# Performance work log

Hardware: AMD Instinct MI355X
Metric: run time of the kernel (lower is better)

The kernel has to match this reference:

```python
import jax, jax.numpy as jnp
import numpy as np

N = 100000
E = 1600000
G = 128


def _degrees(src, dst, n):
    ones = jnp.ones(src.shape[0], dtype=jnp.float32)
    deg_out = jax.ops.segment_sum(ones, src, num_segments=n)
    deg_in = jax.ops.segment_sum(ones, dst, num_segments=n)
    return jnp.maximum(deg_out, 1.0), jnp.maximum(deg_in, 1.0)


def gcn_conv(x, W, b, src, dst, norm_out, norm_in):
    # DGL GraphConv, norm='both': scale src by d_out^-1/2, sum over edges,
    # scale dst by d_in^-1/2, then linear. Weight applied first (out<=in) --
    # mathematically identical, cheaper gather.
    h = (x * norm_out[:, None]) @ W          # [N, out]
    m = h[src]                               # [E, out] gather
    agg = jax.ops.segment_sum(m, dst, num_segments=N)  # [N, out] scatter-add
    return agg * norm_in[:, None] + b


def setup_inputs() -> dict:
    key = jax.random.key(0)
    ks = jax.random.split(key, 8)
    x = jax.random.normal(ks[0], (N, 128), dtype=jnp.float32)
    W1 = jax.random.normal(ks[1], (128, 64), dtype=jnp.float32) * (1.0 / np.sqrt(128))
    b1 = jnp.zeros((64,), dtype=jnp.float32)
    W2 = jax.random.normal(ks[2], (64, 16), dtype=jnp.float32) * (1.0 / np.sqrt(64))
    b2 = jnp.zeros((16,), dtype=jnp.float32)
    src = jax.random.randint(ks[3], (E,), 0, N, dtype=jnp.int32)
    dst = jax.random.randint(ks[4], (E,), 0, N, dtype=jnp.int32)
    graph_ids = jnp.sort(jax.random.randint(ks[5], (N,), 0, G, dtype=jnp.int32))
    return {"x": x, "W1": W1, "b1": b1, "W2": W2, "b2": b2,
            "src": src, "dst": dst, "graph_ids": graph_ids}


def reference(x, W1, b1, W2, b2, src, dst, graph_ids):
    deg_out, deg_in = _degrees(src, dst, N)
    norm_out = jax.lax.rsqrt(deg_out)
    norm_in = jax.lax.rsqrt(deg_in)
    h = gcn_conv(x, W1, b1, src, dst, norm_out, norm_in)
    h = jax.nn.relu(h)
    # dropout(p=0.2) is identity in eval mode
    h = gcn_conv(h, W2, b2, src, dst, norm_out, norm_in)
    # dgl.mean_nodes: per-graph mean pooling
    sums = jax.ops.segment_sum(h, graph_ids, num_segments=G)      # [G, 16]
    counts = jax.ops.segment_sum(jnp.ones((N,), jnp.float32), graph_ids, num_segments=G)
    return sums / jnp.maximum(counts, 1.0)[:, None]
```

## Files before the change

kernel.cpp:

```cpp
#include <hip/hip_runtime.h>
#include <hip/hip_fp16.h>

#define N_NODES 100000
#define N_EDGES 1600000
#define N_GRAPHS 128
#define SB 391
#define CAP 4608
#define NBLK 512
#define NE4 (N_EDGES / 4)
#define CH4 782
#define LDX 136

typedef unsigned long long u64;
typedef unsigned int u32;
typedef unsigned char u8;
typedef _Float16 f16;
typedef f16 half8 __attribute__((ext_vector_type(8)));
typedef f16 half4v __attribute__((ext_vector_type(4)));
typedef float floatx4 __attribute__((ext_vector_type(4)));

__global__ void k_init(int* __restrict__ cur_d, int* __restrict__ cur_s) {
  int t = blockIdx.x * blockDim.x + threadIdx.x;
  if (t < SB) { cur_d[t] = t * CAP; cur_s[t] = t * CAP; }
}

__global__ __launch_bounds__(256) void k_fuse(const int4* __restrict__ src4,
                                              const int4* __restrict__ dst4,
                                              int* __restrict__ cur_d,
                                              int* __restrict__ cur_s,
                                              u32* __restrict__ ed,
                                              u8* __restrict__ ssk8) {
  __shared__ int hd[SB], hs[SB], ld[SB], ls[SB];
  const int t = threadIdx.x, b = blockIdx.x;
  for (int j = t; j < SB; j += 256) { hd[j] = 0; hs[j] = 0; }
  __syncthreads();
  const int start = b * CH4, end = min(start + CH4, NE4);
  for (int i = start + t; i < end; i += 256) {
    int4 d = dst4[i]; int4 s = src4[i];
    atomicAdd(&hd[d.x >> 8], 1); atomicAdd(&hd[d.y >> 8], 1);
    atomicAdd(&hd[d.z >> 8], 1); atomicAdd(&hd[d.w >> 8], 1);
    atomicAdd(&hs[s.x >> 8], 1); atomicAdd(&hs[s.y >> 8], 1);
    atomicAdd(&hs[s.z >> 8], 1); atomicAdd(&hs[s.w >> 8], 1);
  }
  __syncthreads();
  for (int j = t; j < SB; j += 256) {
    ld[j] = atomicAdd(&cur_d[j], hd[j]);
    ls[j] = atomicAdd(&cur_s[j], hs[j]);
  }
  __syncthreads();
  for (int i = start + t; i < end; i += 256) {
    int4 d4 = dst4[i]; int4 s4 = src4[i];
    {
      int d = d4.x, s = s4.x;
      int pd = atomicAdd(&ld[d >> 8], 1);
      ed[pd] = ((u32)(d & 255) << 24) | (u32)s;
      int ps = atomicAdd(&ls[s >> 8], 1);
      ssk8[ps] = (u8)(s & 255);
    }
    {
      int d = d4.y, s = s4.y;
      int pd = atomicAdd(&ld[d >> 8], 1);
      ed[pd] = ((u32)(d & 255) << 24) | (u32)s;
      int ps = atomicAdd(&ls[s >> 8], 1);
      ssk8[ps] = (u8)(s & 255);
    }
    {
      int d = d4.z, s = s4.z;
      int pd = atomicAdd(&ld[d >> 8], 1);
      ed[pd] = ((u32)(d & 255) << 24) | (u32)s;
      int ps = atomicAdd(&ls[s >> 8], 1);
      ssk8[ps] = (u8)(s & 255);
    }
    {
      int d = d4.w, s = s4.w;
      int pd = atomicAdd(&ld[d >> 8], 1);
      ed[pd] = ((u32)(d & 255) << 24) | (u32)s;
      int ps = atomicAdd(&ls[s >> 8], 1);
      ssk8[ps] = (u8)(s & 255);
    }
  }
}

__global__ __launch_bounds__(256) void k_bucket_csr(const u32* __restrict__ ed,
                                                    const u8* __restrict__ ssk8,
                                                    const int* __restrict__ cur_d,
                                                    const int* __restrict__ cur_s,
                                                    int* __restrict__ row_ptr,
                                                    int* __restrict__ deg,
                                                    float* __restrict__ norm_in,
                                                    float* __restrict__ norm_out,
                                                    int* __restrict__ edge_src) {
  __shared__ int hist[256], scanbuf[256], cursor[256], hist2[256];
  const int b = blockIdx.x, t = threadIdx.x;
  const int base = b << 8;
  const int lo = b * CAP;
  const int hiD = cur_d[b];
  const int hiS = cur_s[b];
  hist[t] = 0; hist2[t] = 0;
  __syncthreads();
  for (int i = lo + t; i < hiS; i += 256) atomicAdd(&hist2[ssk8[i]], 1);
  for (int i = lo + t; i < hiD; i += 256) atomicAdd(&hist[ed[i] >> 24], 1);
  __syncthreads();
  int node = base + t;
  if (node < N_NODES)
    norm_out[node] = rsqrtf(fmaxf((float)hist2[t], 1.0f));
  int v = hist[t];
  scanbuf[t] = v;
  __syncthreads();
  for (int off = 1; off < 256; off <<= 1) {
    int a = (t >= off) ? scanbuf[t - off] : 0;
    __syncthreads(); scanbuf[t] += a; __syncthreads();
  }
  int excl = scanbuf[t] - v;
  if (node < N_NODES) {
    row_ptr[node] = lo + excl;
    deg[node] = v;
    norm_in[node] = rsqrtf(fmaxf((float)v, 1.0f));
  }
  cursor[t] = excl;
  __syncthreads();
  for (int i = lo + t; i < hiD; i += 256) {
    u32 e = ed[i];
    int p = atomicAdd(&cursor[e >> 24], 1);
    edge_src[lo + p] = (int)(e & 0x00FFFFFFu);
  }
}

__global__ __launch_bounds__(256) void k_gemm1(const float* __restrict__ x,
                                               const float* __restrict__ W1,
                                               const float* __restrict__ norm_out,
                                               __half* __restrict__ h1h) {
  __shared__ __align__(16) f16 Xs[64 * LDX];
  __shared__ __align__(16) f16 Ws[64 * LDX];
  const int t = threadIdx.x;
  const int row0 = blockIdx.x * 64;

  const float4* W4 = (const float4*)W1;
  for (int i = t; i < 2048; i += 256) {
    int k = i >> 4, n4 = (i & 15) * 4;
    float4 v = W4[i];
    Ws[(n4 + 0) * LDX + k] = (f16)v.x;
    Ws[(n4 + 1) * LDX + k] = (f16)v.y;
    Ws[(n4 + 2) * LDX + k] = (f16)v.z;
    Ws[(n4 + 3) * LDX + k] = (f16)v.w;
  }
  const float4* x4 = (const float4*)x;
  #pragma unroll
  for (int i = 0; i < 8; ++i) {
    int idx = t + 256 * i;
    int r = idx >> 5, c4 = idx & 31;
    int row = row0 + r;
    float4 v = make_float4(0.f, 0.f, 0.f, 0.f);
    if (row < N_NODES) {
      float s = norm_out[row];
      v = x4[(size_t)row * 32 + c4];
      v.x *= s; v.y *= s; v.z *= s; v.w *= s;
    }
    half4v h = { (f16)v.x, (f16)v.y, (f16)v.z, (f16)v.w };
    *(half4v*)&Xs[r * LDX + c4 * 4] = h;
  }
  __syncthreads();

  const int w = t >> 6, l = t & 63;
  const int m = l & 15, quad = l >> 4;
  floatx4 c0 = {0.f,0.f,0.f,0.f}, c1 = {0.f,0.f,0.f,0.f};
  floatx4 c2 = {0.f,0.f,0.f,0.f}, c3 = {0.f,0.f,0.f,0.f};
  const f16* xrow = &Xs[(w * 16 + m) * LDX + quad * 8];
  const f16* wrow = &Ws[m * LDX + quad * 8];
  #pragma unroll
  for (int kb = 0; kb < 4; ++kb) {
    half8 a  = *(const half8*)(xrow + kb * 32);
    half8 b0 = *(const half8*)(wrow + kb * 32);
    half8 b1 = *(const half8*)(wrow + 16 * LDX + kb * 32);
    half8 b2 = *(const half8*)(wrow + 32 * LDX + kb * 32);
    half8 b3 = *(const half8*)(wrow + 48 * LDX + kb * 32);
    c0 = __builtin_amdgcn_mfma_f32_16x16x32_f16(a, b0, c0, 0, 0, 0);
    c1 = __builtin_amdgcn_mfma_f32_16x16x32_f16(a, b1, c1, 0, 0, 0);
    c2 = __builtin_amdgcn_mfma_f32_16x16x32_f16(a, b2, c2, 0, 0, 0);
    c3 = __builtin_amdgcn_mfma_f32_16x16x32_f16(a, b3, c3, 0, 0, 0);
  }
  #pragma unroll
  for (int r = 0; r < 4; ++r) {
    int row = row0 + w * 16 + quad * 4 + r;
    if (row < N_NODES + 1) {
      __half* dst = h1h + (size_t)row * 64 + m;
      dst[0]  = __float2half(c0[r]);
      dst[16] = __float2half(c1[r]);
      dst[32] = __float2half(c2[r]);
      dst[48] = __float2half(c3[r]);
    }
  }
}

__global__ __launch_bounds__(256) void k_gather_l1(const int* __restrict__ row_ptr,
                                                   const int* __restrict__ deg,
                                                   const int* __restrict__ edge_src,
                                                   const __half* __restrict__ h1h,
                                                   const float* __restrict__ norm_in,
                                                   const float* __restrict__ norm_out,
                                                   const float* __restrict__ b1,
                                                   const float* __restrict__ W2,
                                                   __half* __restrict__ h2h) {
  __shared__ float W2s[64 * 17];
  const int t = threadIdx.x;
  for (int i = t; i < 64 * 16; i += 256) W2s[(i >> 4) * 17 + (i & 15)] = W2[i];
  if (blockIdx.x == 0 && t < 16) h2h[(size_t)N_NODES * 16 + t] = __float2half(0.f);
  __syncthreads();

  const int w = t >> 6;
  const int l = t & 63;
  const int n = blockIdx.x * 4 + w;
  const int hf = l >> 5;
  const u32 c = (u32)(l & 31);

  const u32* __restrict__ h1u = (const u32*)h1h;
  const int lo = row_ptr[n], hi = lo + deg[n];

  float2 a0 = {0.f,0.f}, a1 = {0.f,0.f}, a2 = {0.f,0.f}, a3 = {0.f,0.f};
  float2 a4 = {0.f,0.f}, a5 = {0.f,0.f}, a6 = {0.f,0.f}, a7 = {0.f,0.f};
  for (int i = lo; i < hi; i += 16) {
    int idx = i + (l & 15);
    int sv = (idx < hi) ? edge_src[idx] : (int)N_NODES;
    int s0 = __shfl(sv,  0 + hf, 64);
    int s1 = __shfl(sv,  2 + hf, 64);
    int s2 = __shfl(sv,  4 + hf, 64);
    int s3 = __shfl(sv,  6 + hf, 64);
    int s4 = __shfl(sv,  8 + hf, 64);
    int s5 = __shfl(sv, 10 + hf, 64);
    int s6 = __shfl(sv, 12 + hf, 64);
    int s7 = __shfl(sv, 14 + hf, 64);
    u32 v0 = h1u[(u32)s0 * 32u + c];
    u32 v1 = h1u[(u32)s1 * 32u + c];
    u32 v2 = h1u[(u32)s2 * 32u + c];
    u32 v3 = h1u[(u32)s3 * 32u + c];
    u32 v4 = h1u[(u32)s4 * 32u + c];
    u32 v5 = h1u[(u32)s5 * 32u + c];
    u32 v6 = h1u[(u32)s6 * 32u + c];
    u32 v7 = h1u[(u32)s7 * 32u + c];
    float2 f;
    f = __half22float2(*(__half2*)&v0); a0.x += f.x; a0.y += f.y;
    f = __half22float2(*(__half2*)&v1); a1.x += f.x; a1.y += f.y;
    f = __half22float2(*(__half2*)&v2); a2.x += f.x; a2.y += f.y;
    f = __half22float2(*(__half2*)&v3); a3.x += f.x; a3.y += f.y;
    f = __half22float2(*(__half2*)&v4); a4.x += f.x; a4.y += f.y;
    f = __half22float2(*(__half2*)&v5); a5.x += f.x; a5.y += f.y;
    f = __half22float2(*(__half2*)&v6); a6.x += f.x; a6.y += f.y;
    f = __half22float2(*(__half2*)&v7); a7.x += f.x; a7.y += f.y;
  }
  float accx = ((a0.x + a1.x) + (a2.x + a3.x)) + ((a4.x + a5.x) + (a6.x + a7.x));
  float accy = ((a0.y + a1.y) + (a2.y + a3.y)) + ((a4.y + a5.y) + (a6.y + a7.y));
  accx += __shfl_xor(accx, 32, 64);
  accy += __shfl_xor(accy, 32, 64);

  const float ni = norm_in[n];
  const float2 bb = ((const float2*)b1)[c];
  float h1x = fmaxf(accx * ni + bb.x, 0.0f);
  float h1y = fmaxf(accy * ni + bb.y, 0.0f);

  const int j = l & 15, p = l >> 4;
  float partial = 0.f;
  #pragma unroll
  for (int kk = 0; kk < 16; kk += 2) {
    int sl = p * 8 + (kk >> 1);
    float vx = __shfl(h1x, sl, 64);
    float vy = __shfl(h1y, sl, 64);
    partial += vx * W2s[(p * 16 + kk) * 17 + j];
    partial += vy * W2s[(p * 16 + kk + 1) * 17 + j];
  }
  partial += __shfl_xor(partial, 16, 64);
  partial += __shfl_xor(partial, 32, 64);
  if (l < 16) h2h[(size_t)n * 16 + l] = __float2half(norm_out[n] * partial);
}

__global__ __launch_bounds__(256) void k_gather_l2(const int* __restrict__ row_ptr,
                                                   const int* __restrict__ deg,
                                                   const int* __restrict__ edge_src,
                                                   const __half* __restrict__ h2h,
                                                   const float* __restrict__ norm_in,
                                                   float* __restrict__ agg2) {
  const int t = threadIdx.x;
  const int w = t >> 6;
  const int l = t & 63;
  const int n = blockIdx.x * 4 + w;
  const int f2 = l & 7;
  const int p = l >> 3;

  const u32* __restrict__ h2u = (const u32*)h2h;
  const int lo = row_ptr[n], hi = lo + deg[n];

  float ax = 0.f, ay = 0.f, bx = 0.f, by = 0.f;
  for (int base = lo; base < hi; base += 16) {
    int i1 = base + p, i2 = base + p + 8;
    int s0 = (i1 < hi) ? edge_src[i1] : (int)N_NODES;
    int s1 = (i2 < hi) ? edge_src[i2] : (int)N_NODES;
    u32 v0 = h2u[(u32)s0 * 8u + (u32)f2];
    u32 v1 = h2u[(u32)s1 * 8u + (u32)f2];
    float2 g0 = __half22float2(*(__half2*)&v0);
    float2 g1 = __half22float2(*(__half2*)&v1);
    ax += g0.x; ay += g0.y;
    bx += g1.x; by += g1.y;
  }
  float sx = ax + bx, sy = ay + by;
  sx += __shfl_xor(sx, 8, 64);  sy += __shfl_xor(sy, 8, 64);
  sx += __shfl_xor(sx, 16, 64); sy += __shfl_xor(sy, 16, 64);
  sx += __shfl_xor(sx, 32, 64); sy += __shfl_xor(sy, 32, 64);
  if (l < 8) {
    float ni = norm_in[n];
    ((float2*)agg2)[(size_t)n * 8 + f2] = make_float2(sx * ni, sy * ni);
  }
}

__global__ __launch_bounds__(256) void k_pool(const float* __restrict__ agg2,
                                              const float* __restrict__ b2,
                                              const int* __restrict__ gid,
                                              float* __restrict__ out) {
  const int g = blockIdx.x;
  __shared__ int s_lo, s_hi;
  if (threadIdx.x == 0) {
    int a = 0, b = N_NODES;
    while (a < b) { int m = (a + b) >> 1; if (gid[m] < g) a = m + 1; else b = m; }
    s_lo = a;
    b = N_NODES;
    while (a < b) { int m = (a + b) >> 1; if (gid[m] < g + 1) a = m + 1; else b = m; }
    s_hi = a;
  }
  __syncthreads();
  const int lo = s_lo, hi = s_hi, cnt = hi - lo;
  const int j = threadIdx.x & 15;
  const int r = threadIdx.x >> 4;
  float acc = 0.f;
  for (int n = lo + r; n < hi; n += 16)
    acc += agg2[(size_t)n * 16 + j];

  __shared__ float red[256];
  red[threadIdx.x] = acc;
  __syncthreads();
  #pragma unroll
  for (int s = 8; s > 0; s >>= 1) {
    if (r < s) red[threadIdx.x] += red[threadIdx.x + s * 16];
    __syncthreads();
  }
  if (r == 0)
    out[g * 16 + j] = (cnt > 0) ? (red[j] / (float)cnt + b2[j]) : 0.0f;
}

extern "C" void kernel_launch(void* const* d_in, const int* in_sizes, int n_in,
                              void* d_out, int out_size, void* d_ws, size_t ws_size,
                              hipStream_t stream) {
  const float* x   = (const float*)d_in[0];
  const float* W1  = (const float*)d_in[1];
  const float* b1  = (const float*)d_in[2];
  const float* W2  = (const float*)d_in[3];
  const float* b2  = (const float*)d_in[4];
  const int*   src = (const int*)d_in[5];
  const int*   dst = (const int*)d_in[6];
  const int*   gid = (const int*)d_in[7];
  float* out = (float*)d_out;

  int* wsi = (int*)d_ws;
  float* wsf = (float*)d_ws;

  float* norm_out = wsf + 0;
  float* norm_in  = wsf + 100000;
  int*   row_ptr  = wsi + 200000;
  int*   deg      = wsi + 300000;
  int*   cur_d    = wsi + 400000;
  int*   cur_s    = wsi + 400400;
  int*   edge_src = wsi + 400800;
  const size_t S  = 2202528;
  u8*    ssk8     = (u8*)(wsi + S);
  u32*   ed       = (u32*)(wsi + S + 450432);
  __half* h1h     = (__half*)(wsi + S);
  __half* h2h     = (__half*)(wsi + S + 3200032);
  float*  agg2    = (float*)(wsi + S);

  const int4* src4 = (const int4*)src;
  const int4* dst4 = (const int4*)dst;

  k_init      <<<2, 256, 0, stream>>>(cur_d, cur_s);
  k_fuse      <<<NBLK, 256, 0, stream>>>(src4, dst4, cur_d, cur_s, ed, ssk8);
  k_bucket_csr<<<SB, 256, 0, stream>>>(ed, ssk8, cur_d, cur_s, row_ptr, deg,
                                       norm_in, norm_out, edge_src);
  k_gemm1     <<<(N_NODES + 64) / 64, 256, 0, stream>>>(x, W1, norm_out, h1h);
  k_gather_l1 <<<N_NODES / 4, 256, 0, stream>>>(row_ptr, deg, edge_src, h1h,
                                                norm_in, norm_out, b1, W2, h2h);
  k_gather_l2 <<<N_NODES / 4, 256, 0, stream>>>(row_ptr, deg, edge_src, h2h,
                                                norm_in, agg2);
  k_pool      <<<N_GRAPHS, 256, 0, stream>>>(agg2, b2, gid, out);
}
```

Baseline: 285.6 us.

## Batch 16 nodes per block in layer-1 gather and use MFMA for W2 projection

Each block of the layer-1 gather now handles 16 nodes, four per wavefront processed sequentially, instead of four. The ReLU'd aggregated features are staged in LDS as fp16, and one wavefront applies the 64x16 W2 projection with two 16x16x32 f16 MFMA instructions, replacing the per-node shuffle-and-FMA matvec. The aim is to amortise W2 loading and cut the shuffle-heavy projection. In exchange there is a block barrier, three wavefronts sit idle during the MFMA, W2 and the intermediate are rounded to fp16, and there is less parallelism per block.

```diff
diff --git a/kernel.cpp b/kernel.cpp
--- a/kernel.cpp
+++ b/kernel.cpp
@@ -17,6 +17,7 @@
 typedef _Float16 f16;
 typedef f16 half8 __attribute__((ext_vector_type(8)));
 typedef f16 half4v __attribute__((ext_vector_type(4)));
+typedef f16 half2v __attribute__((ext_vector_type(2)));
 typedef float floatx4 __attribute__((ext_vector_type(4)));
 
 __global__ void k_init(int* __restrict__ cur_d, int* __restrict__ cur_s) {
@@ -201,75 +202,92 @@
                                                    const float* __restrict__ b1,
                                                    const float* __restrict__ W2,
                                                    __half* __restrict__ h2h) {
-  __shared__ float W2s[64 * 17];
+  __shared__ __align__(16) f16 Rs[16 * 72];
+  __shared__ __align__(16) f16 Ws2[16 * 72];
   const int t = threadIdx.x;
-  for (int i = t; i < 64 * 16; i += 256) W2s[(i >> 4) * 17 + (i & 15)] = W2[i];
+  for (int i = t; i < 1024; i += 256) {
+    int k = i >> 4, n = i & 15;
+    Ws2[n * 72 + k] = (f16)W2[i];
+  }
   if (blockIdx.x == 0 && t < 16) h2h[(size_t)N_NODES * 16 + t] = __float2half(0.f);
-  __syncthreads();
 
   const int w = t >> 6;
   const int l = t & 63;
-  const int n = blockIdx.x * 4 + w;
   const int hf = l >> 5;
   const u32 c = (u32)(l & 31);
 
   const u32* __restrict__ h1u = (const u32*)h1h;
-  const int lo = row_ptr[n], hi = lo + deg[n];
-
-  float2 a0 = {0.f,0.f}, a1 = {0.f,0.f}, a2 = {0.f,0.f}, a3 = {0.f,0.f};
-  float2 a4 = {0.f,0.f}, a5 = {0.f,0.f}, a6 = {0.f,0.f}, a7 = {0.f,0.f};
-  for (int i = lo; i < hi; i += 16) {
-    int idx = i + (l & 15);
-    int sv = (idx < hi) ? edge_src[idx] : (int)N_NODES;
-    int s0 = __shfl(sv,  0 + hf, 64);
-    int s1 = __shfl(sv,  2 + hf, 64);
-    int s2 = __shfl(sv,  4 + hf, 64);
-    int s3 = __shfl(sv,  6 + hf, 64);
-    int s4 = __shfl(sv,  8 + hf, 64);
-    int s5 = __shfl(sv, 10 + hf, 64);
-    int s6 = __shfl(sv, 12 + hf, 64);
-    int s7 = __shfl(sv, 14 + hf, 64);
-    u32 v0 = h1u[(u32)s0 * 32u + c];
-    u32 v1 = h1u[(u32)s1 * 32u + c];
-    u32 v2 = h1u[(u32)s2 * 32u + c];
-    u32 v3 = h1u[(u32)s3 * 32u + c];
-    u32 v4 = h1u[(u32)s4 * 32u + c];
-    u32 v5 = h1u[(u32)s5 * 32u + c];
-    u32 v6 = h1u[(u32)s6 * 32u + c];
-    u32 v7 = h1u[(u32)s7 * 32u + c];
-    float2 f;
-    f = __half22float2(*(__half2*)&v0); a0.x += f.x; a0.y += f.y;
-    f = __half22float2(*(__half2*)&v1); a1.x += f.x; a1.y += f.y;
-    f = __half22float2(*(__half2*)&v2); a2.x += f.x; a2.y += f.y;
-    f = __half22float2(*(__half2*)&v3); a3.x += f.x; a3.y += f.y;
-    f = __half22float2(*(__half2*)&v4); a4.x += f.x; a4.y += f.y;
-    f = __half22float2(*(__half2*)&v5); a5.x += f.x; a5.y += f.y;
-    f = __half22float2(*(__half2*)&v6); a6.x += f.x; a6.y += f.y;
-    f = __half22float2(*(__half2*)&v7); a7.x += f.x; a7.y += f.y;
-  }
-  float accx = ((a0.x + a1.x) + (a2.x + a3.x)) + ((a4.x + a5.x) + (a6.x + a7.x));
-  float accy = ((a0.y + a1.y) + (a2.y + a3.y)) + ((a4.y + a5.y) + (a6.y + a7.y));
-  accx += __shfl_xor(accx, 32, 64);
-  accy += __shfl_xor(accy, 32, 64);
-
-  const float ni = norm_in[n];
   const float2 bb = ((const float2*)b1)[c];
-  float h1x = fmaxf(accx * ni + bb.x, 0.0f);
-  float h1y = fmaxf(accy * ni + bb.y, 0.0f);
-
-  const int j = l & 15, p = l >> 4;
-  float partial = 0.f;
-  #pragma unroll
-  for (int kk = 0; kk < 16; kk += 2) {
-    int sl = p * 8 + (kk >> 1);
-    float vx = __shfl(h1x, sl, 64);
-    float vy = __shfl(h1y, sl, 64);
-    partial += vx * W2s[(p * 16 + kk) * 17 + j];
-    partial += vy * W2s[(p * 16 + kk + 1) * 17 + j];
-  }
-  partial += __shfl_xor(partial, 16, 64);
-  partial += __shfl_xor(partial, 32, 64);
-  if (l < 16) h2h[(size_t)n * 16 + l] = __float2half(norm_out[n] * partial);
+  const int base = blockIdx.x * 16;
+
+  #pragma unroll 1
+  for (int i4 = 0; i4 < 4; ++i4) {
+    const int n = base + w * 4 + i4;
+    const int lo = row_ptr[n], hi = lo + deg[n];
+
+    float2 a0 = {0.f,0.f}, a1 = {0.f,0.f}, a2 = {0.f,0.f}, a3 = {0.f,0.f};
+    float2 a4 = {0.f,0.f}, a5 = {0.f,0.f}, a6 = {0.f,0.f}, a7 = {0.f,0.f};
+    for (int i = lo; i < hi; i += 16) {
+      int idx = i + (l & 15);
+      int sv = (idx < hi) ? edge_src[idx] : (int)N_NODES;
+      int s0 = __shfl(sv,  0 + hf, 64);
+      int s1 = __shfl(sv,  2 + hf, 64);
+      int s2 = __shfl(sv,  4 + hf, 64);
+      int s3 = __shfl(sv,  6 + hf, 64);
+      int s4 = __shfl(sv,  8 + hf, 64);
+      int s5 = __shfl(sv, 10 + hf, 64);
+      int s6 = __shfl(sv, 12 + hf, 64);
+      int s7 = __shfl(sv, 14 + hf, 64);
+      u32 v0 = h1u[(u32)s0 * 32u + c];
+      u32 v1 = h1u[(u32)s1 * 32u + c];
+      u32 v2 = h1u[(u32)s2 * 32u + c];
+      u32 v3 = h1u[(u32)s3 * 32u + c];
+      u32 v4 = h1u[(u32)s4 * 32u + c];
+      u32 v5 = h1u[(u32)s5 * 32u + c];
+      u32 v6 = h1u[(u32)s6 * 32u + c];
+      u32 v7 = h1u[(u32)s7 * 32u + c];
+      float2 f;
+      f = __half22float2(*(__half2*)&v0); a0.x += f.x; a0.y += f.y;
+      f = __half22float2(*(__half2*)&v1); a1.x += f.x; a1.y += f.y;
+      f = __half22float2(*(__half2*)&v2); a2.x += f.x; a2.y += f.y;
+      f = __half22float2(*(__half2*)&v3); a3.x += f.x; a3.y += f.y;
+      f = __half22float2(*(__half2*)&v4); a4.x += f.x; a4.y += f.y;
+      f = __half22float2(*(__half2*)&v5); a5.x += f.x; a5.y += f.y;
+      f = __half22float2(*(__half2*)&v6); a6.x += f.x; a6.y += f.y;
+      f = __half22float2(*(__half2*)&v7); a7.x += f.x; a7.y += f.y;
+    }
+    float accx = ((a0.x + a1.x) + (a2.x + a3.x)) + ((a4.x + a5.x) + (a6.x + a7.x));
+    float accy = ((a0.y + a1.y) + (a2.y + a3.y)) + ((a4.y + a5.y) + (a6.y + a7.y));
+    accx += __shfl_xor(accx, 32, 64);
+    accy += __shfl_xor(accy, 32, 64);
+
+    const float ni = norm_in[n];
+    float h1x = fmaxf(accx * ni + bb.x, 0.0f);
+    float h1y = fmaxf(accy * ni + bb.y, 0.0f);
+    if (l < 32) {
+      half2v hv = { (f16)h1x, (f16)h1y };
+      *(half2v*)&Rs[(w * 4 + i4) * 72 + 2 * (int)c] = hv;
+    }
+  }
+  __syncthreads();
+
+  if (w == 0) {
+    const int m = l & 15, q = l >> 4;
+    const f16* ra = &Rs[m * 72 + q * 8];
+    const f16* rb = &Ws2[m * 72 + q * 8];
+    half8 a0 = *(const half8*)ra;
+    half8 a1 = *(const half8*)(ra + 32);
+    half8 b0 = *(const half8*)rb;
+    half8 b1v = *(const half8*)(rb + 32);
+    floatx4 cc = {0.f,0.f,0.f,0.f};
+    cc = __builtin_amdgcn_mfma_f32_16x16x32_f16(a0, b0, cc, 0, 0, 0);
+    cc = __builtin_amdgcn_mfma_f32_16x16x32_f16(a1, b1v, cc, 0, 0, 0);
+    #pragma unroll
+    for (int r = 0; r < 4; ++r) {
+      int row = base + q * 4 + r;
+      h2h[(size_t)row * 16 + m] = __float2half(cc[r] * norm_out[row]);
+    }
+  }
 }
 
 __global__ __launch_bounds__(256) void k_gather_l2(const int* __restrict__ row_ptr,
@@ -382,8 +400,8 @@
   k_bucket_csr<<<SB, 256, 0, stream>>>(ed, ssk8, cur_d, cur_s, row_ptr, deg,
                                        norm_in, norm_out, edge_src);
   k_gemm1     <<<(N_NODES + 64) / 64, 256, 0, stream>>>(x, W1, norm_out, h1h);
-  k_gather_l1 <<<N_NODES / 4, 256, 0, stream>>>(row_ptr, deg, edge_src, h1h,
-                                                norm_in, norm_out, b1, W2, h2h);
+  k_gather_l1 <<<N_NODES / 16, 256, 0, stream>>>(row_ptr, deg, edge_src, h1h,
+                                                 norm_in, norm_out, b1, W2, h2h);
   k_gather_l2 <<<N_NODES / 4, 256, 0, stream>>>(row_ptr, deg, edge_src, h2h,
                                                 norm_in, agg2);
   k_pool      <<<N_GRAPHS, 256, 0, stream>>>(agg2, b2, gid, out);
```

New measurement: 266.5 us. 6.7% less time.
